# Performance work log

Hardware: AMD Instinct MI355X
Metric: run time of the kernel (lower is better)

The kernel has to match this reference:

```python
import jax, jax.numpy as jnp
import numpy as np

LEAK = 0.2
EPS = 1e-8


def _mod_conv(x, style, weight):
    # x: [B,C,H,W], style: [B,C], weight: [O,C,k,k]
    b, c, h, w = x.shape
    o, _, k, _ = weight.shape
    # per-sample modulation + demodulation (StyleGAN2 style)
    wmod = weight[None] * (style[:, None, :, None, None] + 1.0)  # [B,O,C,k,k]
    d = jax.lax.rsqrt(jnp.sum(wmod * wmod, axis=(2, 3, 4), keepdims=True) + EPS)
    wmod = wmod * d
    pad = (k - 1) // 2  # same padding for stride=1, dilation=1
    xg = x.reshape(1, b * c, h, w)
    wg = wmod.reshape(b * o, c, k, k)
    y = jax.lax.conv_general_dilated(
        xg, wg, window_strides=(1, 1), padding=[(pad, pad), (pad, pad)],
        dimension_numbers=('NCHW', 'OIHW', 'NCHW'), feature_group_count=b)
    return y.reshape(b, o, h, w)


def setup_inputs() -> dict:
    key = jax.random.key(0)
    ks = jax.random.split(key, 8)
    B, LAT, CIN, F, H, W = 8, 512, 256, 256, 64, 64
    K = 3
    kaiming = lambda k, shape, fan_in: jax.random.normal(k, shape, jnp.float32) * np.sqrt(2.0 / fan_in)
    return {
        'x': jax.random.normal(ks[0], (B, CIN, H, W), jnp.float32),
        'istyle': jax.random.normal(ks[1], (B, LAT), jnp.float32),
        'ws1': jax.random.normal(ks[2], (CIN, LAT), jnp.float32) * (1.0 / np.sqrt(LAT)),
        'bs1': jnp.zeros((CIN,), jnp.float32),
        'conv1_w': kaiming(ks[3], (F, CIN, K, K), CIN * K * K),
        'ws2': jax.random.normal(ks[4], (F, LAT), jnp.float32) * (1.0 / np.sqrt(LAT)),
        'bs2': jnp.zeros((F,), jnp.float32),
        'conv2_w': kaiming(ks[5], (F, F, K, K), F * K * K),
    }


def reference(x, istyle, ws1, bs1, conv1_w, ws2, bs2, conv2_w):
    b, c, h, w = x.shape
    # bilinear upsample x2, align_corners=False (half-pixel centers)
    x = jax.image.resize(x, (b, c, 2 * h, 2 * w), method='bilinear')
    s1 = istyle @ ws1.T + bs1
    x = _mod_conv(x, s1, conv1_w)
    x = jax.nn.leaky_relu(x, LEAK)
    s2 = istyle @ ws2.T + bs2
    x = _mod_conv(x, s2, conv2_w)
    return jax.nn.leaky_relu(x, LEAK)
```

## Files before the change

kernel.cpp:

```cpp
#include <hip/hip_runtime.h>

typedef __bf16 bf16x8 __attribute__((ext_vector_type(8)));
typedef float f32x4 __attribute__((ext_vector_type(4)));


__global__ void style_kernel(const float* __restrict__ istyle,
                             const float* __restrict__ ws1, const float* __restrict__ bs1,
                             const float* __restrict__ ws2, const float* __restrict__ bs2,
                             float* __restrict__ sbuf) {
    int b = blockIdx.x;
    int which = blockIdx.y;
    int c = threadIdx.x;
    const float* ws = which ? ws2 : ws1;
    const float* bs = which ? bs2 : bs1;
    __shared__ float st[512];
    for (int i = threadIdx.x; i < 512; i += 256) st[i] = istyle[b * 512 + i];
    __syncthreads();
    float acc = bs[c];
    const float* wr = ws + (size_t)c * 512;
    for (int l = 0; l < 512; ++l) acc += st[l] * wr[l];
    sbuf[((size_t)which * 8 + b) * 256 + c] = acc;
}

__global__ void modw_kernel(const float* __restrict__ w, const float* __restrict__ s,
                            __bf16* __restrict__ wm) {
    int b = blockIdx.x >> 8;
    int o = blockIdx.x & 255;
    int c = threadIdx.x;
    float sm = s[(size_t)b * 256 + c] + 1.0f;
    float v[9];
    float ss = 0.f;
    const float* wr = w + ((size_t)o * 256 + c) * 9;
#pragma unroll
    for (int t = 0; t < 9; ++t) { v[t] = wr[t] * sm; ss += v[t] * v[t]; }
    __shared__ float red[256];
    red[c] = ss;
    __syncthreads();
    for (int sh = 128; sh > 0; sh >>= 1) {
        if (c < sh) red[c] += red[c + sh];
        __syncthreads();
    }
    float d = rsqrtf(red[0] + 1e-8f);
#pragma unroll
    for (int t = 0; t < 9; ++t)
        wm[(((size_t)(b * 256 + o) * 9 + t) * 256) + c] = (__bf16)(v[t] * d);
}

__global__ void zeropad_kernel(__bf16* __restrict__ xu, __bf16* __restrict__ y1) {
    int p = blockIdx.x;
    int b = blockIdx.y;
    __bf16* buf = blockIdx.z ? y1 : xu;
    int y, x;
    if (p < 130)      { y = 0;           x = p; }
    else if (p < 260) { y = 129;         x = p - 130; }
    else if (p < 388) { y = p - 260 + 1; x = 0; }
    else              { y = p - 388 + 1; x = 129; }
    uint4 z = make_uint4(0, 0, 0, 0);
    *(uint4*)(buf + (((size_t)b * 130 + y) * 130 + x) * 256 + threadIdx.x * 8) = z;
}

__global__ void upsample_kernel(const float* __restrict__ x, __bf16* __restrict__ xu) {
    int ct = blockIdx.x;
    int y  = blockIdx.y;
    int b  = blockIdx.z;
    int c0 = ct * 32;
    __shared__ float up[32 * 132];
    int tid = threadIdx.x;

    int j = y >> 1;
    int y0, y1; float wy0, wy1;
    if (y & 1) { y0 = j; y1 = (j + 1 < 64) ? j + 1 : 63; wy0 = 0.75f; wy1 = 0.25f; }
    else       { y0 = (j - 1 >= 0) ? j - 1 : 0; y1 = j; wy0 = 0.25f; wy1 = 0.75f; }

    int c  = tid >> 3;
    int xs = (tid & 7) * 16;
    const float* row0 = x + ((size_t)(b * 256 + c0 + c) * 64 + y0) * 64;
    const float* row1 = x + ((size_t)(b * 256 + c0 + c) * 64 + y1) * 64;
#pragma unroll
    for (int k = 0; k < 16; ++k) {
        int xo = xs + k;
        int i = xo >> 1;
        int x0, x1; float wx0, wx1;
        if (xo & 1) { x0 = i; x1 = (i + 1 < 64) ? i + 1 : 63; wx0 = 0.75f; wx1 = 0.25f; }
        else        { x0 = (i - 1 >= 0) ? i - 1 : 0; x1 = i; wx0 = 0.25f; wx1 = 0.75f; }
        float v0 = wx0 * row0[x0] + wx1 * row0[x1];
        float v1 = wx0 * row1[x0] + wx1 * row1[x1];
        up[c * 132 + xo] = wy0 * v0 + wy1 * v1;
    }
    __syncthreads();
    int xo = tid >> 1, half = tid & 1;
    union { __bf16 v[8]; uint4 u; } pk;
#pragma unroll
    for (int g = 0; g < 2; ++g) {
#pragma unroll
        for (int i = 0; i < 8; ++i)
            pk.v[i] = (__bf16)up[(half * 16 + g * 8 + i) * 132 + xo];
        *(uint4*)(xu + (((size_t)(b * 130) + y + 1) * 130 + xo + 1) * 256 + c0 + half * 16 + g * 8) = pk.u;
    }
}

template <int PHASE>
__global__ __launch_bounds__(256, 3) void conv_kernel(
    const __bf16* __restrict__ in,
    const __bf16* __restrict__ wm,
    float* __restrict__ outf,
    __bf16* __restrict__ outb) {
    __shared__ __bf16 Al[128 * 64];
    __shared__ __bf16 Bl[128 * 64];
    const int tid   = threadIdx.x;
    const int bid   = blockIdx.x;
    const int swz   = (bid & 7) * 256 + (bid >> 3);
    const int b     = swz >> 8;
    const int bx    = swz & 255;
    const int yrow  = bx >> 1;
    const int mtile = bx & 1;
    const int om    = mtile * 128;
    const int lane  = tid & 63;
    const int wv    = tid >> 6;
    const int wo    = (wv >> 1) * 64;
    const int wn    = (wv & 1) * 64;
    const int lr    = lane >> 3;
    const int lc    = lane & 7;
    const int swzc  = (lc ^ lr) * 8;
    const int arow  = lane & 15;
    const int cgb   = lane >> 4;

    const size_t wmbase = ((size_t)(b * 256 + om + wv * 32 + lr) * 9) * 256 + swzc;
    const size_t inbase = (size_t)b * 130 * 130 * 256 + (size_t)(wv * 32 + lr) * 256 + swzc;

    f32x4 acc[4][4] = {};

    for (int tap = 0; tap < 9; ++tap) {
        const int ky = tap / 3, kx = tap % 3;
        const size_t inrow = inbase + (size_t)((yrow + ky) * 130 + kx) * 256;
        const size_t wrow  = wmbase + (size_t)tap * 256;
        for (int c0 = 0; c0 < 256; c0 += 64) {
#pragma unroll
            for (int q = 0; q < 4; ++q) {
                __builtin_amdgcn_global_load_lds(
                    (const __attribute__((address_space(1))) unsigned int*)(wm + wrow + (size_t)q * 8 * 9 * 256 + c0),
                    (__attribute__((address_space(3))) unsigned int*)(Al + (wv * 32 + q * 8) * 64),
                    16, 0, 0);
                __builtin_amdgcn_global_load_lds(
                    (const __attribute__((address_space(1))) unsigned int*)(in + inrow + (size_t)q * 8 * 256 + c0),
                    (__attribute__((address_space(3))) unsigned int*)(Bl + (wv * 32 + q * 8) * 64),
                    16, 0, 0);
            }
            __syncthreads();
#pragma unroll
            for (int ks = 0; ks < 2; ++ks) {
                const int cg = ks * 4 + cgb;
                bf16x8 af[4], bfr[4];
#pragma unroll
                for (int i = 0; i < 4; ++i) {
                    int ra = wo + i * 16 + arow;
                    af[i]  = *(const bf16x8*)((const char*)Al + ra * 128 + ((cg ^ (ra & 7)) * 16));
                    int rb = wn + i * 16 + arow;
                    bfr[i] = *(const bf16x8*)((const char*)Bl + rb * 128 + ((cg ^ (rb & 7)) * 16));
                }
#pragma unroll
                for (int i = 0; i < 4; ++i)
#pragma unroll
                    for (int j = 0; j < 4; ++j)
                        acc[i][j] = __builtin_amdgcn_mfma_f32_16x16x32_bf16(af[i], bfr[j], acc[i][j], 0, 0, 0);
            }
            __syncthreads();
        }
    }

#pragma unroll
    for (int i = 0; i < 4; ++i) {
#pragma unroll
        for (int j = 0; j < 4; ++j) {
            int o_base = om + wo + i * 16 + (lane >> 4) * 4;
            int n      = wn + j * 16 + (lane & 15);
            if (PHASE == 1) {
                union { __bf16 v[4]; uint2 u; } pk;
#pragma unroll
                for (int r = 0; r < 4; ++r) {
                    float t = acc[i][j][r];
                    t = (t > 0.f) ? t : 0.2f * t;
                    pk.v[r] = (__bf16)t;
                }
                *(uint2*)(outb + (((size_t)(b * 130) + yrow + 1) * 130 + n + 1) * 256 + o_base) = pk.u;
            } else {
#pragma unroll
                for (int r = 0; r < 4; ++r) {
                    float t = acc[i][j][r];
                    t = (t > 0.f) ? t : 0.2f * t;
                    outf[(((size_t)b * 256 + o_base + r) * 128 + yrow) * 128 + n] = t;
                }
            }
        }
    }
}

extern "C" void kernel_launch(void* const* d_in, const int* in_sizes, int n_in,
                              void* d_out, int out_size, void* d_ws, size_t ws_size,
                              hipStream_t stream) {
    const float* x      = (const float*)d_in[0];
    const float* istyle = (const float*)d_in[1];
    const float* ws1    = (const float*)d_in[2];
    const float* bs1    = (const float*)d_in[3];
    const float* w1     = (const float*)d_in[4];
    const float* ws2    = (const float*)d_in[5];
    const float* bs2    = (const float*)d_in[6];
    const float* w2     = (const float*)d_in[7];
    float* out = (float*)d_out;

    char* ws = (char*)d_ws;
    __bf16* xu_p = (__bf16*)(ws);
    __bf16* y1_p = (__bf16*)(ws + 69222400);
    __bf16* wm   = (__bf16*)(ws + 138444800);
    float*  sbuf = (float*)(ws + 147881984);

    style_kernel<<<dim3(8, 2), 256, 0, stream>>>(istyle, ws1, bs1, ws2, bs2, sbuf);
    zeropad_kernel<<<dim3(516, 8, 2), 32, 0, stream>>>(xu_p, y1_p);
    upsample_kernel<<<dim3(8, 128, 8), 256, 0, stream>>>(x, xu_p);
    modw_kernel<<<dim3(2048), 256, 0, stream>>>(w1, sbuf, wm);
    conv_kernel<1><<<dim3(2048), 256, 0, stream>>>(xu_p, wm, nullptr, y1_p);
    modw_kernel<<<dim3(2048), 256, 0, stream>>>(w2, sbuf + 2048, wm);
    conv_kernel<2><<<dim3(2048), 256, 0, stream>>>(y1_p, wm, out, nullptr);
}
```

Before: 418.2 us.

## Double-buffer conv LDS loads, stage phase-1 output via LDS, streamline modw and zeropad

The conv kernel now double-buffers its A/B tiles in LDS, issuing global-to-LDS loads for the next K-step while MFMAs run on the current one. It flattens the tap and channel loops into 36 steps, raises MFMA priority with setprio, and drops occupancy from 3 to 2 blocks per CU to fit 64KB of LDS. The phase-1 epilogue goes through swizzled LDS so the bf16 NHWC stores are 16-byte coalesced. modw switches to one wave per (b,o) with a shuffle reduction, and zeropad packs 8 pixels per block. The trade-off is lower occupancy and a single vmcnt(0) barrier per step.

```diff
diff --git a/kernel.cpp b/kernel.cpp
--- a/kernel.cpp
+++ b/kernel.cpp
@@ -3,6 +3,12 @@
 typedef __bf16 bf16x8 __attribute__((ext_vector_type(8)));
 typedef float f32x4 __attribute__((ext_vector_type(4)));
 
+
+#define GLDS(gsrc, ldst) __builtin_amdgcn_global_load_lds( \
+    (const __attribute__((address_space(1))) unsigned int*)(gsrc), \
+    (__attribute__((address_space(3))) unsigned int*)(ldst), 16, 0, 0)
+
+#define MFMA(a, b, c) __builtin_amdgcn_mfma_f32_16x16x32_bf16((a), (b), (c), 0, 0, 0)
 
 __global__ void style_kernel(const float* __restrict__ istyle,
                              const float* __restrict__ ws1, const float* __restrict__ bs1,
@@ -24,39 +30,51 @@
 
 __global__ void modw_kernel(const float* __restrict__ w, const float* __restrict__ s,
                             __bf16* __restrict__ wm) {
-    int b = blockIdx.x >> 8;
-    int o = blockIdx.x & 255;
-    int c = threadIdx.x;
-    float sm = s[(size_t)b * 256 + c] + 1.0f;
-    float v[9];
+    int wv = threadIdx.x >> 6, lane = threadIdx.x & 63;
+    int idx = blockIdx.x * 4 + wv;
+    int b = idx >> 8, o = idx & 255;
+    int c0 = lane * 4;
+    const float* wr = w + ((size_t)o * 256 + c0) * 9;
+    const float* sb = s + (size_t)b * 256 + c0;
+    float v[36];
     float ss = 0.f;
-    const float* wr = w + ((size_t)o * 256 + c) * 9;
-#pragma unroll
-    for (int t = 0; t < 9; ++t) { v[t] = wr[t] * sm; ss += v[t] * v[t]; }
-    __shared__ float red[256];
-    red[c] = ss;
-    __syncthreads();
-    for (int sh = 128; sh > 0; sh >>= 1) {
-        if (c < sh) red[c] += red[c + sh];
-        __syncthreads();
-    }
-    float d = rsqrtf(red[0] + 1e-8f);
-#pragma unroll
-    for (int t = 0; t < 9; ++t)
-        wm[(((size_t)(b * 256 + o) * 9 + t) * 256) + c] = (__bf16)(v[t] * d);
+#pragma unroll
+    for (int cc = 0; cc < 4; ++cc) {
+        float sm = sb[cc] + 1.0f;
+#pragma unroll
+        for (int t = 0; t < 9; ++t) {
+            float x = wr[cc * 9 + t] * sm;
+            v[cc * 9 + t] = x;
+            ss += x * x;
+        }
+    }
+#pragma unroll
+    for (int off = 32; off > 0; off >>= 1) ss += __shfl_xor(ss, off);
+    float d = rsqrtf(ss + 1e-8f);
+    __bf16* wp = wm + ((size_t)(b * 256 + o) * 9) * 256 + c0;
+#pragma unroll
+    for (int t = 0; t < 9; ++t) {
+        union { __bf16 h[4]; uint2 u; } pk;
+#pragma unroll
+        for (int cc = 0; cc < 4; ++cc) pk.h[cc] = (__bf16)(v[cc * 9 + t] * d);
+        *(uint2*)(wp + (size_t)t * 256) = pk.u;
+    }
 }
 
 __global__ void zeropad_kernel(__bf16* __restrict__ xu, __bf16* __restrict__ y1) {
-    int p = blockIdx.x;
-    int b = blockIdx.y;
+    int p0 = blockIdx.x * 8;
+    int b  = blockIdx.y;
     __bf16* buf = blockIdx.z ? y1 : xu;
+    int p = p0 + (threadIdx.x >> 5);
+    if (p >= 516) return;
+    int chunk = threadIdx.x & 31;
     int y, x;
     if (p < 130)      { y = 0;           x = p; }
     else if (p < 260) { y = 129;         x = p - 130; }
     else if (p < 388) { y = p - 260 + 1; x = 0; }
     else              { y = p - 388 + 1; x = 129; }
     uint4 z = make_uint4(0, 0, 0, 0);
-    *(uint4*)(buf + (((size_t)b * 130 + y) * 130 + x) * 256 + threadIdx.x * 8) = z;
+    *(uint4*)(buf + (((size_t)b * 130 + y) * 130 + x) * 256 + chunk * 8) = z;
 }
 
 __global__ void upsample_kernel(const float* __restrict__ x, __bf16* __restrict__ xu) {
@@ -100,98 +118,144 @@
 }
 
 template <int PHASE>
-__global__ __launch_bounds__(256, 3) void conv_kernel(
+__global__ __launch_bounds__(256, 2) void conv_kernel(
     const __bf16* __restrict__ in,
-    const __bf16* __restrict__ wm,
+    const __bf16* __restrict__ wmall,
     float* __restrict__ outf,
     __bf16* __restrict__ outb) {
-    __shared__ __bf16 Al[128 * 64];
-    __shared__ __bf16 Bl[128 * 64];
-    const int tid   = threadIdx.x;
-    const int bid   = blockIdx.x;
-    const int swz   = (bid & 7) * 256 + (bid >> 3);
-    const int b     = swz >> 8;
-    const int bx    = swz & 255;
-    const int yrow  = bx >> 1;
-    const int mtile = bx & 1;
-    const int om    = mtile * 128;
-    const int lane  = tid & 63;
-    const int wv    = tid >> 6;
-    const int wo    = (wv >> 1) * 64;
-    const int wn    = (wv & 1) * 64;
-    const int lr    = lane >> 3;
-    const int lc    = lane & 7;
-    const int swzc  = (lc ^ lr) * 8;
-    const int arow  = lane & 15;
-    const int cgb   = lane >> 4;
-
-    const size_t wmbase = ((size_t)(b * 256 + om + wv * 32 + lr) * 9) * 256 + swzc;
-    const size_t inbase = (size_t)b * 130 * 130 * 256 + (size_t)(wv * 32 + lr) * 256 + swzc;
+    __shared__ __attribute__((aligned(128))) char smem[65536];
+    __bf16* const sA = (__bf16*)smem;
+    __bf16* const sB = (__bf16*)(smem + 32768);
+    const int tid  = threadIdx.x;
+    const int bid  = blockIdx.x;
+    const int swz  = (bid & 7) * 256 + (bid >> 3);
+    const int b    = swz >> 8;
+    const int rem  = swz & 255;
+    const int yrow = rem >> 1;
+    const int om   = (rem & 1) * 128;
+    const int lane = tid & 63;
+    const int wv   = tid >> 6;
+    const int wo   = (wv >> 1) * 64;
+    const int wn   = (wv & 1) * 64;
+    const int arow = lane & 15;
+    const int cgb  = lane >> 4;
+    const int lr   = lane >> 3;
+    const int lc   = lane & 7;
+    const int swz8 = (lc ^ lr) * 8;
+    const __bf16* wm_b = wmall + (size_t)(b * 256 + om) * 2304;
+
+    size_t aOff[4], bOff[4];
+    int dst[4];
+#pragma unroll
+    for (int q = 0; q < 4; ++q) {
+        int r = q * 32 + wv * 8 + lr;
+        aOff[q] = (size_t)r * 2304 + swz8;
+        bOff[q] = ((size_t)((b * 130 + yrow) * 130 + r)) * 256 + swz8;
+        dst[q]  = (q * 32 + wv * 8) * 64;
+    }
 
     f32x4 acc[4][4] = {};
 
-    for (int tap = 0; tap < 9; ++tap) {
-        const int ky = tap / 3, kx = tap % 3;
-        const size_t inrow = inbase + (size_t)((yrow + ky) * 130 + kx) * 256;
-        const size_t wrow  = wmbase + (size_t)tap * 256;
-        for (int c0 = 0; c0 < 256; c0 += 64) {
+#pragma unroll
+    for (int q = 0; q < 4; ++q) {
+        GLDS(wm_b + aOff[q], sA + dst[q]);
+        GLDS(in   + bOff[q], sB + dst[q]);
+    }
+    asm volatile("s_waitcnt vmcnt(0)" ::: "memory");
+    __builtin_amdgcn_s_barrier();
+    asm volatile("" ::: "memory");
+
+    for (int t = 0; t < 36; ++t) {
+        const __bf16* Ac = sA + (t & 1) * 8192;
+        const __bf16* Bc = sB + (t & 1) * 8192;
+        __bf16* An = sA + ((t + 1) & 1) * 8192;
+        __bf16* Bn = sB + ((t + 1) & 1) * 8192;
+        if (t < 35) {
+            const int nt   = t + 1;
+            const int ncb  = nt / 9;
+            const int ntap = nt - 9 * ncb;
+            const int nc0  = ncb * 64;
+            const int nky  = ntap / 3, nkx = ntap - 3 * nky;
+            const size_t boff_t = (size_t)((nky * 130 + nkx) * 256 + nc0);
+            const size_t aoff_t = (size_t)(ntap * 256 + nc0);
 #pragma unroll
             for (int q = 0; q < 4; ++q) {
-                __builtin_amdgcn_global_load_lds(
-                    (const __attribute__((address_space(1))) unsigned int*)(wm + wrow + (size_t)q * 8 * 9 * 256 + c0),
-                    (__attribute__((address_space(3))) unsigned int*)(Al + (wv * 32 + q * 8) * 64),
-                    16, 0, 0);
-                __builtin_amdgcn_global_load_lds(
-                    (const __attribute__((address_space(1))) unsigned int*)(in + inrow + (size_t)q * 8 * 256 + c0),
-                    (__attribute__((address_space(3))) unsigned int*)(Bl + (wv * 32 + q * 8) * 64),
-                    16, 0, 0);
-            }
-            __syncthreads();
-#pragma unroll
-            for (int ks = 0; ks < 2; ++ks) {
-                const int cg = ks * 4 + cgb;
-                bf16x8 af[4], bfr[4];
-#pragma unroll
-                for (int i = 0; i < 4; ++i) {
-                    int ra = wo + i * 16 + arow;
-                    af[i]  = *(const bf16x8*)((const char*)Al + ra * 128 + ((cg ^ (ra & 7)) * 16));
-                    int rb = wn + i * 16 + arow;
-                    bfr[i] = *(const bf16x8*)((const char*)Bl + rb * 128 + ((cg ^ (rb & 7)) * 16));
+                GLDS(wm_b + aOff[q] + aoff_t, An + dst[q]);
+                GLDS(in   + bOff[q] + boff_t, Bn + dst[q]);
+            }
+        }
+        bf16x8 bfr[4][2], af[4][2];
+#pragma unroll
+        for (int j = 0; j < 4; ++j) {
+            int rb = wn + j * 16 + arow;
+            const char* bp = (const char*)Bc + rb * 128;
+            bfr[j][0] = *(const bf16x8*)(bp + ((cgb ^ (rb & 7)) * 16));
+            bfr[j][1] = *(const bf16x8*)(bp + (((cgb + 4) ^ (rb & 7)) * 16));
+        }
+#pragma unroll
+        for (int m = 0; m < 4; ++m) {
+            int ra = wo + m * 16 + arow;
+            const char* ap = (const char*)Ac + ra * 128;
+            af[m][0] = *(const bf16x8*)(ap + ((cgb ^ (ra & 7)) * 16));
+            af[m][1] = *(const bf16x8*)(ap + (((cgb + 4) ^ (ra & 7)) * 16));
+        }
+        __builtin_amdgcn_s_setprio(1);
+#pragma unroll
+        for (int m = 0; m < 4; ++m)
+#pragma unroll
+            for (int j = 0; j < 4; ++j) {
+                acc[m][j] = MFMA(af[m][0], bfr[j][0], acc[m][j]);
+                acc[m][j] = MFMA(af[m][1], bfr[j][1], acc[m][j]);
+            }
+        __builtin_amdgcn_s_setprio(0);
+        asm volatile("s_waitcnt vmcnt(0)" ::: "memory");
+        __builtin_amdgcn_s_barrier();
+        asm volatile("" ::: "memory");
+    }
+
+    __builtin_amdgcn_sched_barrier(0);
+    __syncthreads();
+
+    if (PHASE == 1) {
+        __bf16* const ot = (__bf16*)smem;
+        const int cg = lane >> 4;
+#pragma unroll
+        for (int m = 0; m < 4; ++m)
+#pragma unroll
+            for (int j = 0; j < 4; ++j) {
+                int n  = wn + j * 16 + arow;
+                int ob = (wo + m * 16 + cg * 4) * 2;
+                union { __bf16 v[4]; uint2 u; } pk;
+#pragma unroll
+                for (int r = 0; r < 4; ++r) {
+                    float v = acc[m][j][r];
+                    pk.v[r] = (__bf16)((v > 0.f) ? v : 0.2f * v);
                 }
-#pragma unroll
-                for (int i = 0; i < 4; ++i)
-#pragma unroll
-                    for (int j = 0; j < 4; ++j)
-                        acc[i][j] = __builtin_amdgcn_mfma_f32_16x16x32_bf16(af[i], bfr[j], acc[i][j], 0, 0, 0);
-            }
-            __syncthreads();
-        }
-    }
-
-#pragma unroll
-    for (int i = 0; i < 4; ++i) {
-#pragma unroll
-        for (int j = 0; j < 4; ++j) {
-            int o_base = om + wo + i * 16 + (lane >> 4) * 4;
-            int n      = wn + j * 16 + (lane & 15);
-            if (PHASE == 1) {
-                union { __bf16 v[4]; uint2 u; } pk;
+                *(uint2*)((char*)ot + n * 256 + (ob ^ ((n & 7) << 4))) = pk.u;
+            }
+        __syncthreads();
+        const int p4  = lane >> 4;
+        const int c16 = lane & 15;
+#pragma unroll
+        for (int it = 0; it < 8; ++it) {
+            int n = wv * 32 + it * 4 + p4;
+            uint4 v = *(const uint4*)((const char*)ot + n * 256 + ((c16 * 16) ^ ((n & 7) << 4)));
+            *(uint4*)(outb + (((size_t)(b * 130) + yrow + 1) * 130 + n + 1) * 256 + om + c16 * 8) = v;
+        }
+    } else {
+#pragma unroll
+        for (int m = 0; m < 4; ++m)
+#pragma unroll
+            for (int j = 0; j < 4; ++j) {
+                int o_base = om + wo + m * 16 + (lane >> 4) * 4;
+                int n      = wn + j * 16 + (lane & 15);
 #pragma unroll
                 for (int r = 0; r < 4; ++r) {
-                    float t = acc[i][j][r];
-                    t = (t > 0.f) ? t : 0.2f * t;
-                    pk.v[r] = (__bf16)t;
+                    float v = acc[m][j][r];
+                    v = (v > 0.f) ? v : 0.2f * v;
+                    outf[((size_t)(b * 256 + o_base + r) * 128 + yrow) * 128 + n] = v;
                 }
-                *(uint2*)(outb + (((size_t)(b * 130) + yrow + 1) * 130 + n + 1) * 256 + o_base) = pk.u;
-            } else {
-#pragma unroll
-                for (int r = 0; r < 4; ++r) {
-                    float t = acc[i][j][r];
-                    t = (t > 0.f) ? t : 0.2f * t;
-                    outf[(((size_t)b * 256 + o_base + r) * 128 + yrow) * 128 + n] = t;
-                }
-            }
-        }
+            }
     }
 }
 
@@ -215,10 +279,10 @@
     float*  sbuf = (float*)(ws + 147881984);
 
     style_kernel<<<dim3(8, 2), 256, 0, stream>>>(istyle, ws1, bs1, ws2, bs2, sbuf);
-    zeropad_kernel<<<dim3(516, 8, 2), 32, 0, stream>>>(xu_p, y1_p);
+    zeropad_kernel<<<dim3(65, 8, 2), 256, 0, stream>>>(xu_p, y1_p);
     upsample_kernel<<<dim3(8, 128, 8), 256, 0, stream>>>(x, xu_p);
-    modw_kernel<<<dim3(2048), 256, 0, stream>>>(w1, sbuf, wm);
+    modw_kernel<<<dim3(512), 256, 0, stream>>>(w1, sbuf, wm);
     conv_kernel<1><<<dim3(2048), 256, 0, stream>>>(xu_p, wm, nullptr, y1_p);
-    modw_kernel<<<dim3(2048), 256, 0, stream>>>(w2, sbuf + 2048, wm);
+    modw_kernel<<<dim3(512), 256, 0, stream>>>(w2, sbuf + 2048, wm);
     conv_kernel<2><<<dim3(2048), 256, 0, stream>>>(y1_p, wm, out, nullptr);
 }
```

Result: faster. 398.4 us (-4.7%).
